# Kernel optimization log

Hardware: AMD Instinct MI355X
Metric: run time of the kernel (lower is better)

## Reference

```python
import jax, jax.numpy as jnp
import numpy as np

N, E = 20000, 320000
IN_F, H, D = 1280, 4, 128
HD = H * D  # 512
NEG_SLOPE = 0.2


def setup_inputs() -> dict:
    key = jax.random.key(0)
    ks = jax.random.split(key, 16)
    feature = jax.random.normal(ks[0], (1, N, IN_F), dtype=jnp.float32)
    src = jax.random.randint(ks[1], (E,), 0, N, dtype=jnp.int32)
    dst = jnp.sort(jax.random.randint(ks[2], (E,), 0, N, dtype=jnp.int32))
    s1 = 1.0 / np.sqrt(IN_F)
    s2 = 1.0 / np.sqrt(HD)
    W1 = jax.random.normal(ks[3], (IN_F, HD), dtype=jnp.float32) * s1
    al1 = jax.random.normal(ks[4], (H, D), dtype=jnp.float32) * s2
    ar1 = jax.random.normal(ks[5], (H, D), dtype=jnp.float32) * s2
    b1 = jnp.zeros((HD,), dtype=jnp.float32)
    W2 = jax.random.normal(ks[6], (HD, HD), dtype=jnp.float32) * s2
    al2 = jax.random.normal(ks[7], (H, D), dtype=jnp.float32) * s2
    ar2 = jax.random.normal(ks[8], (H, D), dtype=jnp.float32) * s2
    b2 = jnp.zeros((HD,), dtype=jnp.float32)
    Wfc = jax.random.normal(ks[9], (HD, 64), dtype=jnp.float32) * s2
    bfc = jnp.zeros((64,), dtype=jnp.float32)
    return dict(feature=feature, src=src, dst=dst, W1=W1, al1=al1, ar1=ar1,
                b1=b1, W2=W2, al2=al2, ar2=ar2, b2=b2, Wfc=Wfc, bfc=bfc)


def gat_conv(x, src, dst, W, al, ar, b):
    # x: (N, F_in) -> (N, H, D). DGL GATConv math, negative_slope=0.2.
    h = (x @ W).reshape(N, H, D)
    el = jnp.sum(h * al, axis=-1)                       # (N, H)
    er = jnp.sum(h * ar, axis=-1)                       # (N, H)
    e = jax.nn.leaky_relu(el[src] + er[dst], NEG_SLOPE)  # (E, H)
    # edge softmax segmented by destination node
    m = jax.ops.segment_max(e, dst, num_segments=N, indices_are_sorted=True)
    ex = jnp.exp(e - m[dst])                            # (E, H)
    denom = jax.ops.segment_sum(ex, dst, num_segments=N, indices_are_sorted=True)
    alpha = ex / denom[dst]                             # (E, H)
    out = jax.ops.segment_sum(alpha[:, :, None] * h[src], dst,
                              num_segments=N, indices_are_sorted=True)  # (N,H,D)
    return out + b.reshape(H, D)


def reference(feature, src, dst, W1, al1, ar1, b1, W2, al2, ar2, b2, Wfc, bfc):
    x = feature[0]                                      # squeeze(0) -> (N, 1280)
    out = gat_conv(x, src, dst, W1, al1, ar1, b1)
    out = jax.nn.elu(out).reshape(N, HD)
    out = gat_conv(out, src, dst, W2, al2, ar2, b2)
    out = jax.nn.elu(out).reshape(N, HD)
    out = out @ Wfc + bfc                               # (N, 64)
    out = jax.nn.elu(out[None])                         # (1, N, 64)
    return out
```

## Files before the change

kernel.cpp:

```cpp
#include <hip/hip_runtime.h>
#include <hip/hip_bf16.h>
#include <math.h>

typedef __bf16 bf16_t;
typedef __bf16 bf16x8 __attribute__((ext_vector_type(8)));
typedef float f32x4 __attribute__((ext_vector_type(4)));

__device__ __forceinline__ void gload_lds16(const void* g, void* l) {
  __builtin_amdgcn_global_load_lds((const __attribute__((address_space(1))) void*)g,
                                   (__attribute__((address_space(3))) void*)l, 16, 0, 0);
}

__global__ void castk(const float* __restrict__ in, bf16_t* __restrict__ out, int n) {
  int i = (blockIdx.x * blockDim.x + threadIdx.x) * 8;
  if (i >= n) return;
  float4 a = *(const float4*)(in + i);
  float4 b = *(const float4*)(in + i + 4);
  bf16x8 o;
  o[0] = (bf16_t)a.x; o[1] = (bf16_t)a.y; o[2] = (bf16_t)a.z; o[3] = (bf16_t)a.w;
  o[4] = (bf16_t)b.x; o[5] = (bf16_t)b.y; o[6] = (bf16_t)b.z; o[7] = (bf16_t)b.w;
  *(bf16x8*)(out + i) = o;
}

__global__ void transk(const float* __restrict__ in, bf16_t* __restrict__ out,
                       int K, int N) {
  __shared__ float t[32][33];
  int n0 = blockIdx.x * 32, k0 = blockIdx.y * 32;
  int tx = threadIdx.x & 31, ty = threadIdx.x >> 5;
#pragma unroll
  for (int r = ty; r < 32; r += 8) t[r][tx] = in[(size_t)(k0 + r) * N + n0 + tx];
  __syncthreads();
#pragma unroll
  for (int r = ty; r < 32; r += 8)
    out[(size_t)(n0 + r) * K + k0 + tx] = (bf16_t)t[tx][r];
}

__global__ void rowoffk(const int* __restrict__ dst, int* __restrict__ ro, int N, int E) {
  int n = blockIdx.x * blockDim.x + threadIdx.x;
  if (n > N) return;
  if (n == N) { ro[N] = E; return; }
  int lo = 0, hi = E;
  while (lo < hi) { int mid = (lo + hi) >> 1; if (dst[mid] < n) lo = mid + 1; else hi = mid; }
  ro[n] = lo;
}

__global__ void elerk(const bf16_t* __restrict__ Hb, const float* __restrict__ al,
                      const float* __restrict__ ar, float* __restrict__ el,
                      float* __restrict__ er, int N) {
  int node = blockIdx.x * 4 + (threadIdx.x >> 6);
  int lane = threadIdx.x & 63;
  if (node >= N) return;
  bf16x8 v = *(const bf16x8*)(Hb + (size_t)node * 512 + lane * 8);
  int head = lane >> 4;
  int dbase = (lane & 15) * 8;
  float sl = 0.f, sr = 0.f;
#pragma unroll
  for (int t = 0; t < 8; t++) {
    float f = (float)v[t];
    sl += f * al[head * 128 + dbase + t];
    sr += f * ar[head * 128 + dbase + t];
  }
#pragma unroll
  for (int off = 1; off < 16; off <<= 1) {
    sl += __shfl_xor(sl, off);
    sr += __shfl_xor(sr, off);
  }
  if ((lane & 15) == 0) {
    el[node * 4 + head] = sl;
    er[node * 4 + head] = sr;
  }
}

__global__ void edgek(const float* __restrict__ el, const float* __restrict__ er,
                      const int* __restrict__ src, const int* __restrict__ dst,
                      float* __restrict__ pw, int E) {
  int e = blockIdx.x * blockDim.x + threadIdx.x;
  if (e >= E) return;
  int s = src[e], d = dst[e];
  float4 ev = *(const float4*)(el + (size_t)s * 4);
  float4 rv = *(const float4*)(er + (size_t)d * 4);
  float c;
  c = ev.x + rv.x; c = c >= 0.f ? c : 0.2f * c; pw[e] = __expf(c);
  c = ev.y + rv.y; c = c >= 0.f ? c : 0.2f * c; pw[(size_t)E + e] = __expf(c);
  c = ev.z + rv.z; c = c >= 0.f ? c : 0.2f * c; pw[(size_t)2 * E + e] = __expf(c);
  c = ev.w + rv.w; c = c >= 0.f ? c : 0.2f * c; pw[(size_t)3 * E + e] = __expf(c);
}

#define GK_NPB 32
__global__ __launch_bounds__(256) void gatherk(
    const bf16_t* __restrict__ Hb, const float* __restrict__ pw,
    const int* __restrict__ src, const int* __restrict__ ro,
    const float* __restrict__ bias, bf16_t* __restrict__ out, int N, int E) {
  const int slice = blockIdx.x & 7;
  const int group = blockIdx.x >> 3;
  const int w = threadIdx.x >> 6, lane = threadIdx.x & 63;
  const int g = lane >> 3;
  const int oct = lane & 7;
  const int head = slice >> 1;
  const float* __restrict__ ph = pw + (size_t)head * E;
  const int dimbase = slice * 64 + oct * 8;

  const int n = group * GK_NPB + w * 8 + g;
  const int e0 = ro[n], e1 = ro[n + 1];

  float acc[8] = {0.f, 0.f, 0.f, 0.f, 0.f, 0.f, 0.f, 0.f};
  float psum = 0.f;

  for (int eb = e0 & ~7; eb < e1; eb += 8) {
    const int4 sv0 = *(const int4*)(src + eb);
    const int4 sv1 = *(const int4*)(src + eb + 4);
    const float4 pv0 = *(const float4*)(ph + eb);
    const float4 pv1 = *(const float4*)(ph + eb + 4);
    int ss[8]; float pp[8];
    ss[0] = sv0.x; ss[1] = sv0.y; ss[2] = sv0.z; ss[3] = sv0.w;
    ss[4] = sv1.x; ss[5] = sv1.y; ss[6] = sv1.z; ss[7] = sv1.w;
    pp[0] = pv0.x; pp[1] = pv0.y; pp[2] = pv0.z; pp[3] = pv0.w;
    pp[4] = pv1.x; pp[5] = pv1.y; pp[6] = pv1.z; pp[7] = pv1.w;
#pragma unroll
    for (int j = 0; j < 8; j++) {
      const int e = eb + j;
      if (e < e0 || e >= e1) pp[j] = 0.f;
    }
    bf16x8 v[8];
#pragma unroll
    for (int j = 0; j < 8; j++)
      v[j] = *(const bf16x8*)(Hb + (size_t)ss[j] * 512 + dimbase);
#pragma unroll
    for (int j = 0; j < 8; j++) {
      psum += pp[j];
#pragma unroll
      for (int t = 0; t < 8; t++) acc[t] += pp[j] * (float)v[j][t];
    }
  }

  const float ih = psum > 0.f ? 1.0f / psum : 0.f;
  const float4 b0 = *(const float4*)(bias + dimbase);
  const float4 b1 = *(const float4*)(bias + dimbase + 4);
  bf16x8 o; float vv;
  vv = acc[0] * ih + b0.x; o[0] = (bf16_t)(vv > 0.f ? vv : expm1f(vv));
  vv = acc[1] * ih + b0.y; o[1] = (bf16_t)(vv > 0.f ? vv : expm1f(vv));
  vv = acc[2] * ih + b0.z; o[2] = (bf16_t)(vv > 0.f ? vv : expm1f(vv));
  vv = acc[3] * ih + b0.w; o[3] = (bf16_t)(vv > 0.f ? vv : expm1f(vv));
  vv = acc[4] * ih + b1.x; o[4] = (bf16_t)(vv > 0.f ? vv : expm1f(vv));
  vv = acc[5] * ih + b1.y; o[5] = (bf16_t)(vv > 0.f ? vv : expm1f(vv));
  vv = acc[6] * ih + b1.z; o[6] = (bf16_t)(vv > 0.f ? vv : expm1f(vv));
  vv = acc[7] * ih + b1.w; o[7] = (bf16_t)(vv > 0.f ? vv : expm1f(vv));
  *(bf16x8*)(out + (size_t)n * 512 + dimbase) = o;
}

template <int BM, int BN, int WM, int WN, int EPI>
__global__ __launch_bounds__(256) void gemm_bt(
    const bf16_t* __restrict__ A, const bf16_t* __restrict__ Bt,
    void* __restrict__ C, const float* __restrict__ bias,
    int M, int N, int K) {
  constexpr int BK = 32;
  constexpr int WTM = BM / WM, WTN = BN / WN;
  constexpr int MF = WTM / 16, NF = WTN / 16;

  __shared__ bf16_t sA[BM][BK];
  __shared__ bf16_t sB[BN][BK];

  const int tid = threadIdx.x;
  const int wid = tid >> 6, lane = tid & 63;
  const int wr = wid / WN, wc = wid % WN;

  const int nby = N / BN;
  const int nwg = gridDim.x;
  const int q = nwg >> 3, r = nwg & 7;
  const int xcd = blockIdx.x & 7, pos = blockIdx.x >> 3;
  const int wg = (xcd < r ? xcd * (q + 1) : r * (q + 1) + (xcd - r) * q) + pos;
  const int row0 = (wg / nby) * BM;
  const int col0 = (wg % nby) * BN;

  f32x4 acc[MF][NF];
#pragma unroll
  for (int i = 0; i < MF; i++)
#pragma unroll
    for (int j = 0; j < NF; j++) acc[i][j] = (f32x4){0.f, 0.f, 0.f, 0.f};

  const int lr = lane >> 2;
  const int lkb = (lane & 3) * 8;

  for (int k0 = 0; k0 < K; k0 += BK) {
#pragma unroll
    for (int i = 0; i < BM / 16; i += 4) {
      int r2 = (i + wid) * 16 + lr;
      int grow = row0 + r2; if (grow > M - 1) grow = M - 1;
      gload_lds16(A + (size_t)grow * K + k0 + lkb, &sA[(i + wid) * 16][0]);
    }
#pragma unroll
    for (int i = 0; i < BN / 16; i += 4) {
      int r2 = (i + wid) * 16 + lr;
      gload_lds16(Bt + (size_t)(col0 + r2) * K + k0 + lkb, &sB[(i + wid) * 16][0]);
    }
    __syncthreads();
    bf16x8 af[MF], bfr[NF];
#pragma unroll
    for (int i = 0; i < MF; i++)
      af[i] = *(const bf16x8*)&sA[wr * WTM + i * 16 + (lane & 15)][(lane >> 4) * 8];
#pragma unroll
    for (int j = 0; j < NF; j++)
      bfr[j] = *(const bf16x8*)&sB[wc * WTN + j * 16 + (lane & 15)][(lane >> 4) * 8];
#pragma unroll
    for (int i = 0; i < MF; i++)
#pragma unroll
      for (int j = 0; j < NF; j++)
        acc[i][j] = __builtin_amdgcn_mfma_f32_16x16x32_bf16(af[i], bfr[j], acc[i][j], 0, 0, 0);
    __syncthreads();
  }

#pragma unroll
  for (int i = 0; i < MF; i++) {
#pragma unroll
    for (int j = 0; j < NF; j++) {
#pragma unroll
      for (int rr = 0; rr < 4; rr++) {
        int row = row0 + wr * WTM + i * 16 + (lane >> 4) * 4 + rr;
        int col = col0 + wc * WTN + j * 16 + (lane & 15);
        if (row < M) {
          float v = acc[i][j][rr];
          if constexpr (EPI == 0) {
            ((bf16_t*)C)[(size_t)row * N + col] = (bf16_t)v;
          } else {
            v += bias[col];
            v = v > 0.f ? v : expm1f(v);
            ((float*)C)[(size_t)row * N + col] = v;
          }
        }
      }
    }
  }
}

extern "C" void kernel_launch(void* const* d_in, const int* in_sizes, int n_in,
                              void* d_out, int out_size, void* d_ws, size_t ws_size,
                              hipStream_t stream) {
  const float* feature = (const float*)d_in[0];
  const int* src = (const int*)d_in[1];
  const int* dst = (const int*)d_in[2];
  const float* W1 = (const float*)d_in[3];
  const float* al1 = (const float*)d_in[4];
  const float* ar1 = (const float*)d_in[5];
  const float* b1 = (const float*)d_in[6];
  const float* W2 = (const float*)d_in[7];
  const float* al2 = (const float*)d_in[8];
  const float* ar2 = (const float*)d_in[9];
  const float* b2 = (const float*)d_in[10];
  const float* Wfc = (const float*)d_in[11];
  const float* bfc = (const float*)d_in[12];

  const int N = 20000, E = 320000, INF = 1280, HD = 512;

  char* ws = (char*)d_ws;
  size_t off = 0;
  auto alloc = [&](size_t bytes) {
    void* p = ws + off;
    off += (bytes + 255) & ~(size_t)255;
    return p;
  };
  bf16_t* Xb  = (bf16_t*)alloc((size_t)N * INF * 2);
  bf16_t* W1t = (bf16_t*)alloc((size_t)HD * INF * 2);
  bf16_t* W2t = (bf16_t*)alloc((size_t)HD * HD * 2);
  bf16_t* Wft = (bf16_t*)alloc((size_t)64 * HD * 2);
  bf16_t* Hb  = (bf16_t*)alloc((size_t)N * HD * 2);
  bf16_t* Xn  = (bf16_t*)alloc((size_t)N * HD * 2);
  float* el = (float*)alloc((size_t)N * 4 * 4);
  float* er = (float*)alloc((size_t)N * 4 * 4);
  float* pw = (float*)alloc((size_t)E * 4 * 4);
  int* ro = (int*)alloc((size_t)(N + 1) * 4);

  castk<<<(N * INF) / (256 * 8), 256, 0, stream>>>(feature, Xb, N * INF);
  {
    dim3 g(HD / 32, INF / 32);
    transk<<<g, 256, 0, stream>>>(W1, W1t, INF, HD);
  }
  {
    dim3 g(HD / 32, HD / 32);
    transk<<<g, 256, 0, stream>>>(W2, W2t, HD, HD);
  }
  {
    dim3 g(64 / 32, HD / 32);
    transk<<<g, 256, 0, stream>>>(Wfc, Wft, HD, 64);
  }
  rowoffk<<<(N + 1 + 255) / 256, 256, 0, stream>>>(dst, ro, N, E);

  const int nbx = (N + 127) / 128;
  const int nbxf = (N + 63) / 64;
  const int gatherBlocks = (N / GK_NPB) * 8;
  const int edgeBlocks = (E + 255) / 256;

  gemm_bt<128, 64, 2, 2, 0><<<nbx * (HD / 64), 256, 0, stream>>>(Xb, W1t, Hb, nullptr, N, HD, INF);
  elerk<<<N / 4, 256, 0, stream>>>(Hb, al1, ar1, el, er, N);
  edgek<<<edgeBlocks, 256, 0, stream>>>(el, er, src, dst, pw, E);
  gatherk<<<gatherBlocks, 256, 0, stream>>>(Hb, pw, src, ro, b1, Xn, N, E);

  gemm_bt<128, 64, 2, 2, 0><<<nbx * (HD / 64), 256, 0, stream>>>(Xn, W2t, Hb, nullptr, N, HD, HD);
  elerk<<<N / 4, 256, 0, stream>>>(Hb, al2, ar2, el, er, N);
  edgek<<<edgeBlocks, 256, 0, stream>>>(el, er, src, dst, pw, E);
  gatherk<<<gatherBlocks, 256, 0, stream>>>(Hb, pw, src, ro, b2, Xn, N, E);

  gemm_bt<64, 64, 2, 2, 1><<<nbxf, 256, 0, stream>>>(Xn, Wft, d_out, bfc, N, 64, HD);
}
```

Baseline: 214.0 us.

## Double-buffer GEMM LDS tiles with XOR swizzle, BK=64 and larger tiles

The bf16 MFMA GEMM now double-buffers its shared-memory tiles, so the next K-tile is loaded while the current one is computed. K depth per stage goes from 32 to 64, and an XOR swizzle on the 16-byte chunks is meant to avoid LDS bank conflicts. The two large GEMMs move to 128x128 tiles and the final FC GEMM to 128x64 with a 4x1 warp layout. This raises LDS use and register pressure per block and cuts the grid size, which may lower occupancy and wave fill on the MI355X.

```diff
diff --git a/kernel.cpp b/kernel.cpp
--- a/kernel.cpp
+++ b/kernel.cpp
@@ -153,12 +153,12 @@
     const bf16_t* __restrict__ A, const bf16_t* __restrict__ Bt,
     void* __restrict__ C, const float* __restrict__ bias,
     int M, int N, int K) {
-  constexpr int BK = 32;
+  constexpr int BK = 64;
   constexpr int WTM = BM / WM, WTN = BN / WN;
   constexpr int MF = WTM / 16, NF = WTN / 16;
 
-  __shared__ bf16_t sA[BM][BK];
-  __shared__ bf16_t sB[BN][BK];
+  __shared__ bf16_t sA[2][BM][BK];
+  __shared__ bf16_t sB[2][BN][BK];
 
   const int tid = threadIdx.x;
   const int wid = tid >> 6, lane = tid & 63;
@@ -178,34 +178,57 @@
 #pragma unroll
     for (int j = 0; j < NF; j++) acc[i][j] = (f32x4){0.f, 0.f, 0.f, 0.f};
 
-  const int lr = lane >> 2;
-  const int lkb = (lane & 3) * 8;
-
-  for (int k0 = 0; k0 < K; k0 += BK) {
-#pragma unroll
-    for (int i = 0; i < BM / 16; i += 4) {
-      int r2 = (i + wid) * 16 + lr;
-      int grow = row0 + r2; if (grow > M - 1) grow = M - 1;
-      gload_lds16(A + (size_t)grow * K + k0 + lkb, &sA[(i + wid) * 16][0]);
-    }
-#pragma unroll
-    for (int i = 0; i < BN / 16; i += 4) {
-      int r2 = (i + wid) * 16 + lr;
-      gload_lds16(Bt + (size_t)(col0 + r2) * K + k0 + lkb, &sB[(i + wid) * 16][0]);
-    }
-    __syncthreads();
-    bf16x8 af[MF], bfr[NF];
-#pragma unroll
-    for (int i = 0; i < MF; i++)
-      af[i] = *(const bf16x8*)&sA[wr * WTM + i * 16 + (lane & 15)][(lane >> 4) * 8];
-#pragma unroll
-    for (int j = 0; j < NF; j++)
-      bfr[j] = *(const bf16x8*)&sB[wc * WTN + j * 16 + (lane & 15)][(lane >> 4) * 8];
-#pragma unroll
-    for (int i = 0; i < MF; i++)
-#pragma unroll
-      for (int j = 0; j < NF; j++)
-        acc[i][j] = __builtin_amdgcn_mfma_f32_16x16x32_bf16(af[i], bfr[j], acc[i][j], 0, 0, 0);
+  const int b_r = lane >> 3, b_p = lane & 7;
+
+  auto stage = [&](int st, int k0) {
+#pragma unroll
+    for (int j = 0; j < BM / 32; j++) {
+      const int rj = (j * 4 + wid) * 8;
+      const int row = rj + b_r;
+      int grow = row0 + row; if (grow > M - 1) grow = M - 1;
+      const int s = b_p ^ (row & 7);
+      gload_lds16(A + (size_t)grow * K + k0 + s * 8, &sA[st][rj][0]);
+    }
+#pragma unroll
+    for (int j = 0; j < BN / 32; j++) {
+      const int rj = (j * 4 + wid) * 8;
+      const int row = rj + b_r;
+      const int s = b_p ^ (row & 7);
+      gload_lds16(Bt + (size_t)(col0 + row) * K + k0 + s * 8, &sB[st][rj][0]);
+    }
+  };
+
+  const int NT = K / BK;
+  stage(0, 0);
+  __syncthreads();
+
+  for (int t = 0; t < NT; t++) {
+    const int st = t & 1;
+    if (t + 1 < NT) stage(st ^ 1, (t + 1) * BK);
+
+#pragma unroll
+    for (int kk = 0; kk < BK; kk += 32) {
+      bf16x8 af[MF], bfr[NF];
+#pragma unroll
+      for (int i = 0; i < MF; i++) {
+        const int row = wr * WTM + i * 16 + (lane & 15);
+        const int s = kk / 8 + (lane >> 4);
+        const int p = s ^ (row & 7);
+        af[i] = *(const bf16x8*)&sA[st][row][p * 8];
+      }
+#pragma unroll
+      for (int j = 0; j < NF; j++) {
+        const int row = wc * WTN + j * 16 + (lane & 15);
+        const int s = kk / 8 + (lane >> 4);
+        const int p = s ^ (row & 7);
+        bfr[j] = *(const bf16x8*)&sB[st][row][p * 8];
+      }
+#pragma unroll
+      for (int i = 0; i < MF; i++)
+#pragma unroll
+        for (int j = 0; j < NF; j++)
+          acc[i][j] = __builtin_amdgcn_mfma_f32_16x16x32_bf16(af[i], bfr[j], acc[i][j], 0, 0, 0);
+    }
     __syncthreads();
   }
 
@@ -285,19 +308,20 @@
   rowoffk<<<(N + 1 + 255) / 256, 256, 0, stream>>>(dst, ro, N, E);
 
   const int nbx = (N + 127) / 128;
-  const int nbxf = (N + 63) / 64;
   const int gatherBlocks = (N / GK_NPB) * 8;
   const int edgeBlocks = (E + 255) / 256;
 
-  gemm_bt<128, 64, 2, 2, 0><<<nbx * (HD / 64), 256, 0, stream>>>(Xb, W1t, Hb, nullptr, N, HD, INF);
+  gemm_bt<128, 128, 2, 2, 0><<<nbx * (HD / 128), 256, 0, stream>>>(
+      Xb, W1t, Hb, nullptr, N, HD, INF);
   elerk<<<N / 4, 256, 0, stream>>>(Hb, al1, ar1, el, er, N);
   edgek<<<edgeBlocks, 256, 0, stream>>>(el, er, src, dst, pw, E);
   gatherk<<<gatherBlocks, 256, 0, stream>>>(Hb, pw, src, ro, b1, Xn, N, E);
 
-  gemm_bt<128, 64, 2, 2, 0><<<nbx * (HD / 64), 256, 0, stream>>>(Xn, W2t, Hb, nullptr, N, HD, HD);
+  gemm_bt<128, 128, 2, 2, 0><<<nbx * (HD / 128), 256, 0, stream>>>(
+      Xn, W2t, Hb, nullptr, N, HD, HD);
   elerk<<<N / 4, 256, 0, stream>>>(Hb, al2, ar2, el, er, N);
   edgek<<<edgeBlocks, 256, 0, stream>>>(el, er, src, dst, pw, E);
   gatherk<<<gatherBlocks, 256, 0, stream>>>(Hb, pw, src, ro, b2, Xn, N, E);
 
-  gemm_bt<64, 64, 2, 2, 1><<<nbxf, 256, 0, stream>>>(Xn, Wft, d_out, bfc, N, 64, HD);
-}
+  gemm_bt<128, 64, 4, 1, 1><<<nbx, 256, 0, stream>>>(Xn, Wft, d_out, bfc, N, 64, HD);
+}
```

Result: slower. 221.2 us (+3.4%).
